# Performance work log

Hardware: AMD Instinct MI355X
Metric: run time of the kernel (lower is better)

The kernel has to match this reference:

```python
import jax, jax.numpy as jnp
import numpy as np

B, S, E, H = 32, 1024, 256, 256


def setup_inputs() -> dict:
    key = jax.random.key(0)
    ks = jax.random.split(key, 12)
    sc = 0.02
    return {
        "encoder_inputs": jax.random.normal(ks[0], (B, S, E), jnp.float32),
        "decoder_input": jax.random.normal(ks[1], (B, E), jnp.float32),
        "h0": jax.random.normal(ks[2], (B, H), jnp.float32),
        "c0": jax.random.normal(ks[3], (B, H), jnp.float32),
        "context": jax.random.normal(ks[4], (B, S, H), jnp.float32),
        "W_ih": jax.random.normal(ks[5], (E, 4 * H), jnp.float32) * sc,
        "b_ih": jnp.zeros((4 * H,), jnp.float32),
        "W_hh": jax.random.normal(ks[6], (H, 4 * H), jnp.float32) * sc,
        "b_hh": jnp.zeros((4 * H,), jnp.float32),
        "W_out": jax.random.normal(ks[7], (2 * H, H), jnp.float32) * sc,
        "b_out": jnp.zeros((H,), jnp.float32),
        "Wa_in": jax.random.normal(ks[8], (H, H), jnp.float32) * sc,
        "ba_in": jnp.zeros((H,), jnp.float32),
        "Wa_ctx": jax.random.normal(ks[9], (H, H), jnp.float32) * sc,
        "ba_ctx": jnp.zeros((H,), jnp.float32),
        "v": jax.random.normal(ks[10], (H,), jnp.float32) * sc,
    }


def reference(encoder_inputs, decoder_input, h0, c0, context,
              W_ih, b_ih, W_hh, b_hh, W_out, b_out,
              Wa_in, ba_in, Wa_ctx, ba_ctx, v):
    bsz, seq_len, _ = encoder_inputs.shape
    # Project context once (Attention.context_linear); reused every step.
    ctx_proj = jnp.einsum('bsh,hk->bsk', context, Wa_ctx) + ba_ctx  # [B,S,H]

    def step(carry, _):
        x, h, c, mask = carry  # mask: 1.0 = still available
        gates = x @ W_ih + b_ih + h @ W_hh + b_hh  # [B,4H]
        i, f, g, o = jnp.split(gates, 4, axis=1)   # chunk order: input, forget, cell, out
        c_t = jax.nn.sigmoid(f) * c + jax.nn.sigmoid(i) * jnp.tanh(g)
        h_t = jax.nn.sigmoid(o) * jnp.tanh(c_t)
        # Additive (Bahdanau-style) attention
        inp = h_t @ Wa_in + ba_in                                  # [B,H]
        scores = jnp.einsum('h,bsh->bs', v, jnp.tanh(inp[:, None, :] + ctx_proj))
        scores = jnp.where(mask > 0, scores, -jnp.inf)             # mask selected positions
        alpha = jax.nn.softmax(scores, axis=-1)                    # [B,S]
        attn_hidden = jnp.einsum('bs,bsh->bh', alpha, ctx_proj)    # weighted projected context
        h_out = jnp.tanh(jnp.concatenate([attn_hidden, h_t], axis=1) @ W_out + b_out)
        # Pointer selection + mask/input update
        idx = jnp.argmax(alpha * mask, axis=-1)                    # [B]
        one_ptr = jax.nn.one_hot(idx, seq_len, dtype=mask.dtype)   # [B,S]
        new_mask = mask * (1.0 - one_ptr)
        x_next = jnp.einsum('bs,bse->be', one_ptr, encoder_inputs)
        return (x_next, h_out, c_t, new_mask), (alpha, idx)

    mask0 = jnp.ones((bsz, seq_len), jnp.float32)
    _, (alphas, ptrs) = jax.lax.scan(step, (decoder_input, h0, c0, mask0), None, length=seq_len)
    outputs = jnp.transpose(alphas, (1, 0, 2))  # [B,S,S] attention distribution per step
    pointers = jnp.transpose(ptrs, (1, 0))      # [B,S] selected indices
    return outputs, pointers
```

## Files before the change

### kernel.cpp

```cpp
#include <hip/hip_runtime.h>
#include <math.h>

#define BB 32
#define SSS 1024
#define EE 256
#define HHH 256
#define TEAM 8
#define CHUNK 128
#define NTHR 512
#define CPAD 129
#define THETA 3e-5f
#define MAXCAND 8

#define NEG_INF (-__builtin_huge_valf())

__device__ __forceinline__ double sigd(double x) {
  return 1.0 / (1.0 + exp(-x));
}

__device__ __forceinline__ float fast_tanhf(float x) {
  float e = __expf(2.0f * x);
  return 1.0f - 2.0f * __builtin_amdgcn_rcpf(1.0f + e);
}

__device__ __forceinline__ void gstore(float* p, float v) {
  __hip_atomic_store(p, v, __ATOMIC_RELAXED, __HIP_MEMORY_SCOPE_AGENT);
}
__device__ __forceinline__ float gload(const float* p) {
  return __hip_atomic_load(p, __ATOMIC_RELAXED, __HIP_MEMORY_SCOPE_AGENT);
}
__device__ __forceinline__ void gstored(double* p, double v) {
  __hip_atomic_store(p, v, __ATOMIC_RELAXED, __HIP_MEMORY_SCOPE_AGENT);
}
__device__ __forceinline__ double gloadd(const double* p) {
  return __hip_atomic_load(p, __ATOMIC_RELAXED, __HIP_MEMORY_SCOPE_AGENT);
}

__device__ __forceinline__ void team_bar(int* cnt, int target) {
  __syncthreads();
  if (threadIdx.x == 0) {
    __hip_atomic_fetch_add(cnt, 1, __ATOMIC_RELEASE, __HIP_MEMORY_SCOPE_AGENT);
    while (__hip_atomic_load(cnt, __ATOMIC_RELAXED, __HIP_MEMORY_SCOPE_AGENT) < target) {}
  }
  __syncthreads();
}

__global__ __launch_bounds__(NTHR, 2) void ptrnet(
    const float* __restrict__ enc, const float* __restrict__ dec0,
    const float* __restrict__ h0, const float* __restrict__ c0,
    const float* __restrict__ context,
    const float* __restrict__ W_ih, const float* __restrict__ b_ih,
    const float* __restrict__ W_hh, const float* __restrict__ b_hh,
    const float* __restrict__ W_out, const float* __restrict__ b_out,
    const float* __restrict__ Wa_in, const float* __restrict__ ba_in,
    const float* __restrict__ Wa_ctx, const float* __restrict__ ba_ctx,
    const float* __restrict__ v,
    float* __restrict__ out,
    int* __restrict__ barp,
    float* __restrict__ hbuf, float* __restrict__ htbuf,
    float* __restrict__ pinp, float* __restrict__ stats,
    float* __restrict__ accb, double* __restrict__ refws)
{
  __shared__ __align__(16) float cpT[HHH * CPAD];
  __shared__ double dsc[256];
  __shared__ __align__(8) float ivp[HHH * 2];
  __shared__ double inp_d[HHH];
  __shared__ double gact[128];
  __shared__ float attn_s[HHH];
  __shared__ float ht_s[HHH];
  __shared__ __align__(16) float hx_s[HHH];
  __shared__ __align__(16) float x_s[EE];
  __shared__ float scratch[NTHR];
  __shared__ float bg_s[128];
  __shared__ float bain_s[HHH];
  __shared__ float v_s[HHH];
  __shared__ float score_s[CHUNK];
  __shared__ float w_s[CHUNK];
  __shared__ float alive_s[CHUNK];
  __shared__ float bo_s[32];
  __shared__ float htl_s[32];
  __shared__ double c_d[32];
  __shared__ float scale8_s[TEAM];
  __shared__ float mg_sh, lg_sh, cutoff_sh;
  __shared__ int idx_sh, rf_sh, ncand_sh;
  __shared__ int cand_s[MAXCAND];

  const int tid = threadIdx.x;
  const int b = blockIdx.x & 31;
  const int m = blockIdx.x >> 5;
  int* cnt = barp + b * 32;

  {
    float* raw = cpT;
    const float* ctxp = context + ((size_t)b * SSS + (size_t)m * CHUNK) * HHH;
    for (int i = tid; i < CHUNK * HHH; i += NTHR) raw[i] = ctxp[i];
    __syncthreads();
    const int cc = tid & 255;
    const int rgc = tid >> 8;
    double acc[2][32];
    double bc = (double)ba_ctx[cc];
    for (int half = 0; half < 2; ++half) {
#pragma unroll
      for (int k = 0; k < 32; ++k) acc[half][k] = 0.0;
      for (int h = 0; h < HHH; ++h) {
        double w = (double)Wa_ctx[h * HHH + cc];
        const float* base = &raw[(rgc * 64 + half * 32) * HHH + h];
#pragma unroll
        for (int k = 0; k < 32; ++k) acc[half][k] = fma((double)base[k * HHH], w, acc[half][k]);
      }
    }
    __syncthreads();
#pragma unroll
    for (int half = 0; half < 2; ++half)
#pragma unroll
      for (int k = 0; k < 32; ++k) {
        int row = rgc * 64 + half * 32 + k;
        cpT[cc * CPAD + row] = (float)(acc[half][k] + bc);
      }
  }

  const int q = tid & 127, rg = tid >> 7;
  const int gcol = ((q >> 5) * 256) + m * 32 + (q & 31);
  float w_ih_r[64], w_hh_r[64];
#pragma unroll
  for (int k = 0; k < 64; ++k) {
    w_ih_r[k] = W_ih[(size_t)(rg * 64 + k) * 1024 + gcol];
    w_hh_r[k] = W_hh[(size_t)(rg * 64 + k) * 1024 + gcol];
  }
  const int hp = tid & 255, rh = tid >> 8;
  float w_ain_r[16];
#pragma unroll
  for (int k = 0; k < 16; ++k)
    w_ain_r[k] = Wa_in[(size_t)(m * 32 + rh * 16 + k) * HHH + hp];
  const int c2 = tid & 31, rgo = tid >> 5;
  float w_out_r[32];
#pragma unroll
  for (int k = 0; k < 32; ++k)
    w_out_r[k] = W_out[(size_t)(rgo * 32 + k) * HHH + m * 32 + c2];

  if (tid < 128) {
    int j = ((tid >> 5) * 256) + m * 32 + (tid & 31);
    bg_s[tid] = b_ih[j] + b_hh[j];
    alive_s[tid] = 1.0f;
  }
  if (tid < 256) { bain_s[tid] = ba_in[tid]; v_s[tid] = v[tid]; }
  if (tid < 32)  { bo_s[tid] = b_out[m * 32 + tid]; c_d[tid] = (double)c0[b * HHH + m * 32 + tid]; }
  __syncthreads();

  int bart = 0;

  for (int t = 0; t < SSS; ++t) {
    if (tid < 256) {
      if (t == 0) { x_s[tid] = dec0[b * EE + tid]; hx_s[tid] = h0[b * HHH + tid]; }
      else {
        int ix = idx_sh;
        x_s[tid] = enc[((size_t)b * SSS + ix) * EE + tid];
        hx_s[tid] = gload(&hbuf[b * HHH + tid]);
      }
    }
    __syncthreads();
    {
      float g = 0.0f;
      const float4* x4 = reinterpret_cast<const float4*>(&x_s[rg * 64]);
      const float4* h4 = reinterpret_cast<const float4*>(&hx_s[rg * 64]);
#pragma unroll
      for (int k = 0; k < 16; ++k) {
        float4 xv = x4[k];
        g = fmaf(w_ih_r[4 * k + 0], xv.x, g);
        g = fmaf(w_ih_r[4 * k + 1], xv.y, g);
        g = fmaf(w_ih_r[4 * k + 2], xv.z, g);
        g = fmaf(w_ih_r[4 * k + 3], xv.w, g);
      }
#pragma unroll
      for (int k = 0; k < 16; ++k) {
        float4 hv = h4[k];
        g = fmaf(w_hh_r[4 * k + 0], hv.x, g);
        g = fmaf(w_hh_r[4 * k + 1], hv.y, g);
        g = fmaf(w_hh_r[4 * k + 2], hv.z, g);
        g = fmaf(w_hh_r[4 * k + 3], hv.w, g);
      }
      scratch[tid] = g;
    }
    __syncthreads();
    if (tid < 128) {
      float gsv = scratch[tid] + scratch[128 + tid] + scratch[256 + tid] + scratch[384 + tid] + bg_s[tid];
      double gd = (double)gsv;
      gact[tid] = (tid >= 64 && tid < 96) ? tanh(gd) : sigd(gd);
    }
    __syncthreads();
    if (tid < 32) {
      double cn = gact[32 + tid] * c_d[tid] + gact[tid] * gact[64 + tid];
      double ht = gact[96 + tid] * tanh(cn);
      c_d[tid] = cn;
      float htf = (float)ht;
      htl_s[tid] = htf;
      gstore(&htbuf[b * HHH + m * 32 + tid], htf);
    }
    __syncthreads();
    {
      float p = 0.0f;
#pragma unroll
      for (int k = 0; k < 16; ++k) p = fmaf(w_ain_r[k], htl_s[rh * 16 + k], p);
      scratch[rh * 256 + hp] = p;
    }
    __syncthreads();
    if (tid < 256) gstore(&pinp[((b * TEAM) + m) * HHH + tid], scratch[tid] + scratch[256 + tid]);
    bart += TEAM; team_bar(cnt, bart);

    if (tid < 256) {
      double sd = (double)bain_s[tid];
#pragma unroll
      for (int w = 0; w < TEAM; ++w) sd += (double)gload(&pinp[((b * TEAM) + w) * HHH + tid]);
      inp_d[tid] = sd;
      ivp[2 * tid] = (float)sd; ivp[2 * tid + 1] = v_s[tid];
    }
    __syncthreads();
    {
      const int s = tid & 127, qq = tid >> 7;
      const float* cpc = &cpT[(qq * 64) * CPAD + s];
      const float2* iv = reinterpret_cast<const float2*>(&ivp[2 * qq * 64]);
      float acc0 = 0.0f, acc1 = 0.0f;
#pragma unroll 4
      for (int j = 0; j < 64; j += 2) {
        float2 iv0 = iv[j], iv1 = iv[j + 1];
        float t0 = fast_tanhf(iv0.x + cpc[j * CPAD]);
        float t1 = fast_tanhf(iv1.x + cpc[(j + 1) * CPAD]);
        acc0 = fmaf(iv0.y, t0, acc0);
        acc1 = fmaf(iv1.y, t1, acc1);
      }
      scratch[tid] = acc0 + acc1;
    }
    __syncthreads();
    if (tid < 128)
      score_s[tid] = scratch[tid] + scratch[128 + tid] + scratch[256 + tid] + scratch[384 + tid];
    __syncthreads();
    if (tid < 64) {
      float sa = (alive_s[tid] > 0.0f) ? score_s[tid] : NEG_INF;
      float sb = (alive_s[tid + 64] > 0.0f) ? score_s[tid + 64] : NEG_INF;
      float v1, v2; int i1;
      if (sb > sa) { v1 = sb; i1 = tid + 64; v2 = sa; }
      else         { v1 = sa; i1 = tid;      v2 = sb; }
#pragma unroll
      for (int d = 1; d < 64; d <<= 1) {
        float ov1 = __shfl_xor(v1, d); int oi1 = __shfl_xor(i1, d);
        float ov2 = __shfl_xor(v2, d);
        if (ov1 > v1 || (ov1 == v1 && oi1 < i1)) {
          v2 = fmaxf(v1, ov2); v1 = ov1; i1 = oi1;
        } else {
          v2 = fmaxf(v2, ov1);
        }
      }
      float w0 = (alive_s[tid] > 0.0f) ? __expf(score_s[tid] - v1) : 0.0f;
      float w1 = (alive_s[tid + 64] > 0.0f) ? __expf(score_s[tid + 64] - v1) : 0.0f;
      w_s[tid] = w0; w_s[tid + 64] = w1;
      float l = w0 + w1;
#pragma unroll
      for (int d = 1; d < 64; d <<= 1) l += __shfl_xor(l, d);
      if (tid == 0) {
        float* st = &stats[((b * TEAM) + m) * 4];
        gstore(&st[0], v1);
        gstore(&st[1], l);
        gstore(&st[2], __int_as_float((v1 == NEG_INF) ? 0x7fffffff : (m * CHUNK + i1)));
        gstore(&st[3], v2);
      }
    }
    __syncthreads();
    {
      const int h = tid & 255, sh = tid >> 8;
      const float* cpr = &cpT[h * CPAD + sh * 64];
      const float* wr = &w_s[sh * 64];
      float a = 0.0f;
#pragma unroll 8
      for (int j = 0; j < 64; ++j) a = fmaf(wr[j], cpr[j], a);
      scratch[sh * 256 + h] = a;
    }
    __syncthreads();
    if (tid < 256) gstore(&accb[((b * TEAM) + m) * HHH + tid], scratch[tid] + scratch[256 + tid]);
    bart += TEAM; team_bar(cnt, bart);

    float accp[TEAM]; float htp = 0.0f;
    if (tid < 256) {
#pragma unroll
      for (int w = 0; w < TEAM; ++w) accp[w] = gload(&accb[((b * TEAM) + w) * HHH + tid]);
      htp = gload(&htbuf[b * HHH + tid]);
    }
    if (tid < 32)
      scratch[tid] = gload(&stats[((b * TEAM) + (tid >> 2)) * 4 + (tid & 3)]);
    __syncthreads();
    if (tid == 0) {
      float g1 = NEG_INF, g2 = NEG_INF; int gi = 0x7fffffff;
      float lg = 0.0f;
      float mcv[TEAM], lcv[TEAM];
#pragma unroll
      for (int w = 0; w < TEAM; ++w) {
        mcv[w] = scratch[w * 4 + 0]; lcv[w] = scratch[w * 4 + 1];
        int biv = __float_as_int(scratch[w * 4 + 2]); float v2v = scratch[w * 4 + 3];
        if (lcv[w] > 0.0f) {
          if (mcv[w] > g1 || (mcv[w] == g1 && biv < gi)) {
            g2 = fmaxf(g1, v2v); g1 = mcv[w]; gi = biv;
          } else {
            g2 = fmaxf(g2, mcv[w]);
          }
        }
      }
#pragma unroll
      for (int w = 0; w < TEAM; ++w) {
        float sw = (lcv[w] > 0.0f) ? __expf(mcv[w] - g1) : 0.0f;
        scale8_s[w] = sw; lg += lcv[w] * sw;
      }
      mg_sh = g1; lg_sh = lg; idx_sh = gi;
      rf_sh = (g2 > g1 - THETA) ? 1 : 0;
      cutoff_sh = g1 - THETA;
    }
    __syncthreads();

    if (tid < 128) {
      float sc_ = score_s[tid];
      float al = (alive_s[tid] > 0.0f) ? __expf(sc_ - mg_sh) / lg_sh : 0.0f;
      __builtin_nontemporal_store(al,
          &out[(size_t)b * (SSS * SSS) + (size_t)t * SSS + m * CHUNK + tid]);
    }

    if (rf_sh) {
      if (tid == 0) {
        int nc = 0;
        for (int s2 = 0; s2 < CHUNK; ++s2)
          if (alive_s[s2] > 0.0f && score_s[s2] > cutoff_sh && nc < MAXCAND)
            cand_s[nc++] = s2;
        ncand_sh = nc;
      }
      __syncthreads();
      const int nc = ncand_sh;
      for (int ci = 0; ci < nc; ++ci) {
        const int slot = cand_s[ci];
        if (tid < 256) {
          const float* crow = context + ((size_t)b * SSS + (size_t)(m * CHUNK + slot)) * HHH;
          double acc = (double)ba_ctx[tid];
          for (int h2 = 0; h2 < HHH; ++h2)
            acc = fma((double)crow[h2], (double)Wa_ctx[h2 * HHH + tid], acc);
          double arg = inp_d[tid] + acc;
          dsc[tid] = (double)v_s[tid] * tanh(arg);
        }
        __syncthreads();
        if (tid < 64) {
          double se = dsc[tid] + dsc[tid + 64] + dsc[tid + 128] + dsc[tid + 192];
#pragma unroll
          for (int d = 1; d < 64; d <<= 1) se += __shfl_xor(se, d);
          if (tid == 0) {
            double* rw = &refws[(((size_t)b * TEAM) + m) * (1 + 2 * MAXCAND)];
            gstored(&rw[1 + 2 * ci], (double)(m * CHUNK + slot));
            gstored(&rw[2 + 2 * ci], se);
          }
        }
        __syncthreads();
      }
      if (tid == 0)
        gstored(&refws[(((size_t)b * TEAM) + m) * (1 + 2 * MAXCAND)], (double)nc);
      bart += TEAM; team_bar(cnt, bart);
      if (tid == 0) {
        double bs = -1.0e300; int bi2 = 0x7fffffff;
#pragma unroll
        for (int w = 0; w < TEAM; ++w) {
          const double* rw = &refws[(((size_t)b * TEAM) + w) * (1 + 2 * MAXCAND)];
          int wn = (int)gloadd(&rw[0]);
          for (int j2 = 0; j2 < wn; ++j2) {
            int ii = (int)gloadd(&rw[1 + 2 * j2]); double sv = gloadd(&rw[2 + 2 * j2]);
            if (sv > bs || (sv == bs && ii < bi2)) { bs = sv; bi2 = ii; }
          }
        }
        idx_sh = bi2;
      }
      __syncthreads();
    }

    if (tid < 256) {
      float a = 0.0f;
#pragma unroll
      for (int w = 0; w < TEAM; ++w) a = fmaf(accp[w], scale8_s[w], a);
      attn_s[tid] = a / lg_sh;
      ht_s[tid] = htp;
    }
    __syncthreads();
    {
      float hpart = 0.0f;
#pragma unroll
      for (int k = 0; k < 32; ++k) {
        int r = rgo * 32 + k;
        float vr = (r < 256) ? attn_s[r] : ht_s[r - 256];
        hpart = fmaf(w_out_r[k], vr, hpart);
      }
      scratch[rgo * 32 + c2] = hpart;
    }
    __syncthreads();
    if (tid < 32) {
      float s = bo_s[tid];
#pragma unroll
      for (int j = 0; j < 16; ++j) s += scratch[j * 32 + tid];
      gstore(&hbuf[b * HHH + m * 32 + tid], tanhf(s));
    }
    if (m == 0 && tid == 0)
      __builtin_nontemporal_store((float)idx_sh,
          &out[(size_t)BB * SSS * SSS + (size_t)b * SSS + t]);
    if (tid == 0 && (idx_sh >> 7) == m) alive_s[idx_sh & 127] = 0.0f;
    bart += TEAM; team_bar(cnt, bart);
  }
}

extern "C" void kernel_launch(void* const* d_in, const int* in_sizes, int n_in,
                              void* d_out, int out_size, void* d_ws, size_t ws_size,
                              hipStream_t stream) {
  (void)in_sizes; (void)n_in; (void)out_size; (void)ws_size;
  const float* enc     = (const float*)d_in[0];
  const float* dec0    = (const float*)d_in[1];
  const float* h0      = (const float*)d_in[2];
  const float* c0      = (const float*)d_in[3];
  const float* context = (const float*)d_in[4];
  const float* W_ih    = (const float*)d_in[5];
  const float* b_ih    = (const float*)d_in[6];
  const float* W_hh    = (const float*)d_in[7];
  const float* b_hh    = (const float*)d_in[8];
  const float* W_out   = (const float*)d_in[9];
  const float* b_out   = (const float*)d_in[10];
  const float* Wa_in   = (const float*)d_in[11];
  const float* ba_in   = (const float*)d_in[12];
  const float* Wa_ctx  = (const float*)d_in[13];
  const float* ba_ctx  = (const float*)d_in[14];
  const float* v       = (const float*)d_in[15];

  char* wsb   = (char*)d_ws;
  int*   barp  = (int*)wsb;
  float* hbuf  = (float*)(wsb + 4096);
  float* htbuf = hbuf + 32 * 256;
  float* pinp  = htbuf + 32 * 256;
  float* stats = pinp + 32 * 8 * 256;
  float* accb  = stats + 32 * 8 * 4;
  double* refws = (double*)(accb + 32 * 8 * 256);

  hipMemsetAsync(d_ws, 0, 4096, stream);
  hipLaunchKernelGGL(ptrnet, dim3(256), dim3(NTHR), 0, stream,
                     enc, dec0, h0, c0, context,
                     W_ih, b_ih, W_hh, b_hh, W_out, b_out,
                     Wa_in, ba_in, Wa_ctx, ba_ctx, v,
                     (float*)d_out, barp, hbuf, htbuf, pinp, stats, accb, refws);
}
```

Before: 25.15 ms.

## Split end-of-step barrier into arrive/wait and overlap encoder load; multi-accumulator dots

The end-of-step team barrier becomes a split arrive/wait, so each block prefetches the next encoder row before waiting for the other blocks' hidden state. The LSTM gate activation and cell update are merged into one phase that uses wave shuffles and keeps the cell state in a register, removing a shared array and a sync. Several dot-product loops get multiple independent accumulators for more ILP. The softmax normalisation now uses a reciprocal multiply instead of division. Launch bounds drop to one block per SM, which gives the compiler more registers but may change occupancy.

After: 26.41 ms. 5.0% more time.

```diff
diff --git a/kernel.cpp b/kernel.cpp
--- a/kernel.cpp
+++ b/kernel.cpp
@@ -36,16 +36,23 @@
   return __hip_atomic_load(p, __ATOMIC_RELAXED, __HIP_MEMORY_SCOPE_AGENT);
 }
 
-__device__ __forceinline__ void team_bar(int* cnt, int target) {
+__device__ __forceinline__ void bar_arrive(int* cnt) {
   __syncthreads();
+  if (threadIdx.x == 0)
+    __hip_atomic_fetch_add(cnt, 1, __ATOMIC_RELEASE, __HIP_MEMORY_SCOPE_AGENT);
+}
+__device__ __forceinline__ void bar_wait(int* cnt, int target) {
   if (threadIdx.x == 0) {
-    __hip_atomic_fetch_add(cnt, 1, __ATOMIC_RELEASE, __HIP_MEMORY_SCOPE_AGENT);
     while (__hip_atomic_load(cnt, __ATOMIC_RELAXED, __HIP_MEMORY_SCOPE_AGENT) < target) {}
   }
   __syncthreads();
 }
-
-__global__ __launch_bounds__(NTHR, 2) void ptrnet(
+__device__ __forceinline__ void team_bar(int* cnt, int target) {
+  bar_arrive(cnt);
+  bar_wait(cnt, target);
+}
+
+__global__ __launch_bounds__(NTHR, 1) void ptrnet(
     const float* __restrict__ enc, const float* __restrict__ dec0,
     const float* __restrict__ h0, const float* __restrict__ c0,
     const float* __restrict__ context,
@@ -65,7 +72,6 @@
   __shared__ double dsc[256];
   __shared__ __align__(8) float ivp[HHH * 2];
   __shared__ double inp_d[HHH];
-  __shared__ double gact[128];
   __shared__ float attn_s[HHH];
   __shared__ float ht_s[HHH];
   __shared__ __align__(16) float hx_s[HHH];
@@ -79,9 +85,8 @@
   __shared__ float alive_s[CHUNK];
   __shared__ float bo_s[32];
   __shared__ float htl_s[32];
-  __shared__ double c_d[32];
   __shared__ float scale8_s[TEAM];
-  __shared__ float mg_sh, lg_sh, cutoff_sh;
+  __shared__ float mg_sh, linv_sh, cutoff_sh;
   __shared__ int idx_sh, rf_sh, ncand_sh;
   __shared__ int cand_s[MAXCAND];
 
@@ -144,57 +149,68 @@
     alive_s[tid] = 1.0f;
   }
   if (tid < 256) { bain_s[tid] = ba_in[tid]; v_s[tid] = v[tid]; }
-  if (tid < 32)  { bo_s[tid] = b_out[m * 32 + tid]; c_d[tid] = (double)c0[b * HHH + m * 32 + tid]; }
+  if (tid < 32)  bo_s[tid] = b_out[m * 32 + tid];
+  double c_reg = (tid < 32) ? (double)c0[b * HHH + m * 32 + tid] : 0.0;
   __syncthreads();
 
   int bart = 0;
 
   for (int t = 0; t < SSS; ++t) {
     if (tid < 256) {
-      if (t == 0) { x_s[tid] = dec0[b * EE + tid]; hx_s[tid] = h0[b * HHH + tid]; }
-      else {
-        int ix = idx_sh;
-        x_s[tid] = enc[((size_t)b * SSS + ix) * EE + tid];
-        hx_s[tid] = gload(&hbuf[b * HHH + tid]);
-      }
-    }
+      x_s[tid] = (t == 0) ? dec0[b * EE + tid]
+                          : enc[((size_t)b * SSS + (size_t)idx_sh) * EE + tid];
+    }
+    if (t > 0) bar_wait(cnt, bart);
+    if (tid < 256) hx_s[tid] = (t == 0) ? h0[b * HHH + tid] : gload(&hbuf[b * HHH + tid]);
     __syncthreads();
     {
-      float g = 0.0f;
+      float ax0 = 0.0f, ax1 = 0.0f, ah0 = 0.0f, ah1 = 0.0f;
       const float4* x4 = reinterpret_cast<const float4*>(&x_s[rg * 64]);
       const float4* h4 = reinterpret_cast<const float4*>(&hx_s[rg * 64]);
 #pragma unroll
-      for (int k = 0; k < 16; ++k) {
-        float4 xv = x4[k];
-        g = fmaf(w_ih_r[4 * k + 0], xv.x, g);
-        g = fmaf(w_ih_r[4 * k + 1], xv.y, g);
-        g = fmaf(w_ih_r[4 * k + 2], xv.z, g);
-        g = fmaf(w_ih_r[4 * k + 3], xv.w, g);
-      }
-#pragma unroll
-      for (int k = 0; k < 16; ++k) {
-        float4 hv = h4[k];
-        g = fmaf(w_hh_r[4 * k + 0], hv.x, g);
-        g = fmaf(w_hh_r[4 * k + 1], hv.y, g);
-        g = fmaf(w_hh_r[4 * k + 2], hv.z, g);
-        g = fmaf(w_hh_r[4 * k + 3], hv.w, g);
-      }
-      scratch[tid] = g;
-    }
-    __syncthreads();
-    if (tid < 128) {
-      float gsv = scratch[tid] + scratch[128 + tid] + scratch[256 + tid] + scratch[384 + tid] + bg_s[tid];
-      double gd = (double)gsv;
-      gact[tid] = (tid >= 64 && tid < 96) ? tanh(gd) : sigd(gd);
-    }
-    __syncthreads();
-    if (tid < 32) {
-      double cn = gact[32 + tid] * c_d[tid] + gact[tid] * gact[64 + tid];
-      double ht = gact[96 + tid] * tanh(cn);
-      c_d[tid] = cn;
-      float htf = (float)ht;
-      htl_s[tid] = htf;
-      gstore(&htbuf[b * HHH + m * 32 + tid], htf);
+      for (int k = 0; k < 16; k += 2) {
+        float4 xv0 = x4[k], xv1 = x4[k + 1];
+        ax0 = fmaf(w_ih_r[4 * k + 0], xv0.x, ax0);
+        ax0 = fmaf(w_ih_r[4 * k + 1], xv0.y, ax0);
+        ax0 = fmaf(w_ih_r[4 * k + 2], xv0.z, ax0);
+        ax0 = fmaf(w_ih_r[4 * k + 3], xv0.w, ax0);
+        ax1 = fmaf(w_ih_r[4 * k + 4], xv1.x, ax1);
+        ax1 = fmaf(w_ih_r[4 * k + 5], xv1.y, ax1);
+        ax1 = fmaf(w_ih_r[4 * k + 6], xv1.z, ax1);
+        ax1 = fmaf(w_ih_r[4 * k + 7], xv1.w, ax1);
+      }
+#pragma unroll
+      for (int k = 0; k < 16; k += 2) {
+        float4 hv0 = h4[k], hv1 = h4[k + 1];
+        ah0 = fmaf(w_hh_r[4 * k + 0], hv0.x, ah0);
+        ah0 = fmaf(w_hh_r[4 * k + 1], hv0.y, ah0);
+        ah0 = fmaf(w_hh_r[4 * k + 2], hv0.z, ah0);
+        ah0 = fmaf(w_hh_r[4 * k + 3], hv0.w, ah0);
+        ah1 = fmaf(w_hh_r[4 * k + 4], hv1.x, ah1);
+        ah1 = fmaf(w_hh_r[4 * k + 5], hv1.y, ah1);
+        ah1 = fmaf(w_hh_r[4 * k + 6], hv1.z, ah1);
+        ah1 = fmaf(w_hh_r[4 * k + 7], hv1.w, ah1);
+      }
+      scratch[tid] = (ax0 + ah0) + (ax1 + ah1);
+    }
+    __syncthreads();
+    if (tid < 64) {
+      const int g0 = tid;
+      const int g1 = tid + 64;
+      float s0 = scratch[g0] + scratch[128 + g0] + scratch[256 + g0] + scratch[384 + g0] + bg_s[g0];
+      float s1 = scratch[g1] + scratch[128 + g1] + scratch[256 + g1] + scratch[384 + g1] + bg_s[g1];
+      double act0 = sigd((double)s0);
+      double act1 = (tid < 32) ? tanh((double)s1) : sigd((double)s1);
+      double f_ = __shfl_xor(act0, 32);
+      double o_ = __shfl_xor(act1, 32);
+      if (tid < 32) {
+        double cn = f_ * c_reg + act0 * act1;
+        double ht = o_ * tanh(cn);
+        c_reg = cn;
+        float htf = (float)ht;
+        htl_s[tid] = htf;
+        gstore(&htbuf[b * HHH + m * 32 + tid], htf);
+      }
     }
     __syncthreads();
     {
@@ -219,16 +235,16 @@
       const int s = tid & 127, qq = tid >> 7;
       const float* cpc = &cpT[(qq * 64) * CPAD + s];
       const float2* iv = reinterpret_cast<const float2*>(&ivp[2 * qq * 64]);
-      float acc0 = 0.0f, acc1 = 0.0f;
+      float a0 = 0.0f, a1 = 0.0f, a2 = 0.0f, a3 = 0.0f;
 #pragma unroll 4
-      for (int j = 0; j < 64; j += 2) {
-        float2 iv0 = iv[j], iv1 = iv[j + 1];
-        float t0 = fast_tanhf(iv0.x + cpc[j * CPAD]);
-        float t1 = fast_tanhf(iv1.x + cpc[(j + 1) * CPAD]);
-        acc0 = fmaf(iv0.y, t0, acc0);
-        acc1 = fmaf(iv1.y, t1, acc1);
-      }
-      scratch[tid] = acc0 + acc1;
+      for (int j = 0; j < 64; j += 4) {
+        float2 iv0 = iv[j], iv1 = iv[j + 1], iv2 = iv[j + 2], iv3 = iv[j + 3];
+        a0 = fmaf(iv0.y, fast_tanhf(iv0.x + cpc[(j + 0) * CPAD]), a0);
+        a1 = fmaf(iv1.y, fast_tanhf(iv1.x + cpc[(j + 1) * CPAD]), a1);
+        a2 = fmaf(iv2.y, fast_tanhf(iv2.x + cpc[(j + 2) * CPAD]), a2);
+        a3 = fmaf(iv3.y, fast_tanhf(iv3.x + cpc[(j + 3) * CPAD]), a3);
+      }
+      scratch[tid] = (a0 + a1) + (a2 + a3);
     }
     __syncthreads();
     if (tid < 128)
@@ -269,10 +285,15 @@
       const int h = tid & 255, sh = tid >> 8;
       const float* cpr = &cpT[h * CPAD + sh * 64];
       const float* wr = &w_s[sh * 64];
-      float a = 0.0f;
-#pragma unroll 8
-      for (int j = 0; j < 64; ++j) a = fmaf(wr[j], cpr[j], a);
-      scratch[sh * 256 + h] = a;
+      float a0 = 0.0f, a1 = 0.0f, a2 = 0.0f, a3 = 0.0f;
+#pragma unroll 4
+      for (int j = 0; j < 64; j += 4) {
+        a0 = fmaf(wr[j + 0], cpr[j + 0], a0);
+        a1 = fmaf(wr[j + 1], cpr[j + 1], a1);
+        a2 = fmaf(wr[j + 2], cpr[j + 2], a2);
+        a3 = fmaf(wr[j + 3], cpr[j + 3], a3);
+      }
+      scratch[sh * 256 + h] = (a0 + a1) + (a2 + a3);
     }
     __syncthreads();
     if (tid < 256) gstore(&accb[((b * TEAM) + m) * HHH + tid], scratch[tid] + scratch[256 + tid]);
@@ -289,7 +310,6 @@
     __syncthreads();
     if (tid == 0) {
       float g1 = NEG_INF, g2 = NEG_INF; int gi = 0x7fffffff;
-      float lg = 0.0f;
       float mcv[TEAM], lcv[TEAM];
 #pragma unroll
       for (int w = 0; w < TEAM; ++w) {
@@ -303,12 +323,16 @@
           }
         }
       }
+      float sw[TEAM]; float lg = 0.0f;
 #pragma unroll
       for (int w = 0; w < TEAM; ++w) {
-        float sw = (lcv[w] > 0.0f) ? __expf(mcv[w] - g1) : 0.0f;
-        scale8_s[w] = sw; lg += lcv[w] * sw;
-      }
-      mg_sh = g1; lg_sh = lg; idx_sh = gi;
+        sw[w] = (lcv[w] > 0.0f) ? __expf(mcv[w] - g1) : 0.0f;
+        lg += lcv[w] * sw[w];
+      }
+      float linv = __builtin_amdgcn_rcpf(lg);
+#pragma unroll
+      for (int w = 0; w < TEAM; ++w) scale8_s[w] = sw[w] * linv;
+      mg_sh = g1; linv_sh = linv; idx_sh = gi;
       rf_sh = (g2 > g1 - THETA) ? 1 : 0;
       cutoff_sh = g1 - THETA;
     }
@@ -316,7 +340,7 @@
 
     if (tid < 128) {
       float sc_ = score_s[tid];
-      float al = (alive_s[tid] > 0.0f) ? __expf(sc_ - mg_sh) / lg_sh : 0.0f;
+      float al = (alive_s[tid] > 0.0f) ? __expf(sc_ - mg_sh) * linv_sh : 0.0f;
       __builtin_nontemporal_store(al,
           &out[(size_t)b * (SSS * SSS) + (size_t)t * SSS + m * CHUNK + tid]);
     }
@@ -374,22 +398,25 @@
     }
 
     if (tid < 256) {
-      float a = 0.0f;
-#pragma unroll
-      for (int w = 0; w < TEAM; ++w) a = fmaf(accp[w], scale8_s[w], a);
-      attn_s[tid] = a / lg_sh;
+      float a0 = 0.0f, a1 = 0.0f;
+#pragma unroll
+      for (int w = 0; w < TEAM; w += 2) {
+        a0 = fmaf(accp[w], scale8_s[w], a0);
+        a1 = fmaf(accp[w + 1], scale8_s[w + 1], a1);
+      }
+      attn_s[tid] = a0 + a1;
       ht_s[tid] = htp;
     }
     __syncthreads();
     {
-      float hpart = 0.0f;
-#pragma unroll
-      for (int k = 0; k < 32; ++k) {
-        int r = rgo * 32 + k;
-        float vr = (r < 256) ? attn_s[r] : ht_s[r - 256];
-        hpart = fmaf(w_out_r[k], vr, hpart);
-      }
-      scratch[rgo * 32 + c2] = hpart;
+      const float* srcp = (rgo < 8) ? &attn_s[rgo * 32] : &ht_s[(rgo - 8) * 32];
+      float h0a = 0.0f, h1a = 0.0f;
+#pragma unroll
+      for (int k = 0; k < 32; k += 2) {
+        h0a = fmaf(w_out_r[k], srcp[k], h0a);
+        h1a = fmaf(w_out_r[k + 1], srcp[k + 1], h1a);
+      }
+      scratch[rgo * 32 + c2] = h0a + h1a;
     }
     __syncthreads();
     if (tid < 32) {
@@ -402,7 +429,7 @@
       __builtin_nontemporal_store((float)idx_sh,
           &out[(size_t)BB * SSS * SSS + (size_t)b * SSS + t]);
     if (tid == 0 && (idx_sh >> 7) == m) alive_s[idx_sh & 127] = 0.0f;
-    bart += TEAM; team_bar(cnt, bart);
+    bart += TEAM; bar_arrive(cnt);
   }
 }
 
```
